# Kernel tuning notes

Measured on AMD Instinct MI355X. Metric: run time of the kernel, lower is better.

Reference implementation:

```python
import jax, jax.numpy as jnp
import numpy as np

B, S, I, H = 64, 2048, 256, 512

def setup_inputs() -> dict:
    key = jax.random.key(0)
    k1, k2, k3, k4 = jax.random.split(key, 4)
    stdv = 1.0 / np.sqrt(H)
    return {
        "x": jax.random.normal(k1, (B, S, I), dtype=jnp.float32),
        "W": jax.random.uniform(k2, (I, 3 * H), dtype=jnp.float32, minval=-stdv, maxval=stdv),
        "U": jax.random.uniform(k3, (H, 3 * H), dtype=jnp.float32, minval=-stdv, maxval=stdv),
        "bias": jax.random.uniform(k4, (3 * H,), dtype=jnp.float32, minval=-stdv, maxval=stdv),
    }

def _lstm_noforget(x, W, U, bias):
    # Precompute input projections for all timesteps: (B, S, 3H)
    x_proj = jnp.einsum("bsi,ig->bsg", x, W) + bias
    h0 = jnp.zeros((x.shape[0], H), dtype=x.dtype)
    c0 = jnp.zeros((x.shape[0], H), dtype=x.dtype)

    def step(carry, xp_t):
        h_t, _ = carry
        gates = xp_t + h_t @ U  # (B, 3H)
        i_t = jax.nn.sigmoid(gates[:, :H])
        g_t = jnp.tanh(gates[:, H:2 * H])
        o_t = jax.nn.sigmoid(gates[:, 2 * H:])
        c_t = i_t * g_t          # no-forget: c does not depend on previous c
        h_t = o_t * jnp.tanh(c_t)
        return (h_t, c_t), h_t

    (h_f, c_f), hs = jax.lax.scan(step, (h0, c0), jnp.swapaxes(x_proj, 0, 1))
    hidden_seq = jnp.swapaxes(hs, 0, 1)  # (B, S, H)
    return hidden_seq, h_f, c_f

def reference(x, W, U, bias):
    return _lstm_noforget(x, W, U, bias)
```

## Files before the change

kernel.cpp:

```cpp
#include <hip/hip_runtime.h>
#include <math.h>

#define B_  64
#define S_  2048
#define I_  256
#define H_  512
#define K_  768
#define G3  1536

#define RT  16
#define JT  4
#define NC  12
#define BLK 192
#define LDA 772

__global__ __launch_bounds__(256) void prep_transpose(
    const float* __restrict__ W,
    const float* __restrict__ U,
    float* __restrict__ Vt)
{
    const int c = blockIdx.y;
    const int k = blockIdx.x * 256 + threadIdx.x;
    if (k < K_) {
        float v = (k < I_) ? W[(size_t)k * G3 + c] : U[(size_t)(k - I_) * G3 + c];
        Vt[(size_t)c * K_ + k] = v;
    }
}

__global__ __launch_bounds__(BLK) void lstm_step(
    const float* __restrict__ x,
    const float* __restrict__ bias,
    const float* __restrict__ Vt,
    const float* __restrict__ h_in,
    float* __restrict__ h_out,
    float* __restrict__ hidden,
    float* __restrict__ hf,
    float* __restrict__ cf,
    int t, int is_last)
{
    __shared__ float Alds[RT * LDA];
    __shared__ float gtile[NC][RT + 1];

    const int tid = threadIdx.x;
    const int rq  = blockIdx.x & 3;
    const int jq  = blockIdx.x >> 2;
    const int r0  = rq * RT;

    for (int f4 = tid; f4 < (RT * I_) / 4; f4 += BLK) {
        const int r  = f4 >> 6;
        const int kk = (f4 & 63) * 4;
        const float4 v = *(const float4*)(x + (size_t)(r0 + r) * (S_ * I_) + (size_t)t * I_ + kk);
        *(float4*)(Alds + r * LDA + kk) = v;
    }
    for (int f4 = tid; f4 < (RT * H_) / 4; f4 += BLK) {
        const int r  = f4 >> 7;
        const int jj = (f4 & 127) * 4;
        const float4 v = *(const float4*)(h_in + (size_t)(r0 + r) * H_ + jj);
        *(float4*)(Alds + r * LDA + I_ + jj) = v;
    }
    __syncthreads();

    const int r      = tid & 15;
    const int c      = tid >> 4;
    const int region = c >> 2;
    const int jl     = c & 3;
    const int j      = jq * JT + jl;
    const int cg     = region * H_ + j;

    const float* __restrict__ wrow = Vt + (size_t)cg * K_;
    const float* __restrict__ arow = Alds + r * LDA;

    float4 acc = make_float4(0.f, 0.f, 0.f, 0.f);
    #pragma unroll 4
    for (int k = 0; k < K_; k += 8) {
        const float4 a0 = *(const float4*)(arow + k);
        const float4 a1 = *(const float4*)(arow + k + 4);
        const float4 w0 = *(const float4*)(wrow + k);
        const float4 w1 = *(const float4*)(wrow + k + 4);
        acc.x += a0.x * w0.x;  acc.y += a0.y * w0.y;
        acc.z += a0.z * w0.z;  acc.w += a0.w * w0.w;
        acc.x += a1.x * w1.x;  acc.y += a1.y * w1.y;
        acc.z += a1.z * w1.z;  acc.w += a1.w * w1.w;
    }
    gtile[c][r] = (acc.x + acc.y) + (acc.z + acc.w) + bias[cg];
    __syncthreads();

    if (tid < RT * JT) {
        const int rr = tid & 15;
        const int jj = tid >> 4;
        const float gi = gtile[0 * JT + jj][rr];
        const float gg = gtile[1 * JT + jj][rr];
        const float go = gtile[2 * JT + jj][rr];
        const float it = 1.f / (1.f + __expf(-gi));
        const float gt = tanhf(gg);
        const float ot = 1.f / (1.f + __expf(-go));
        const float ct = it * gt;
        const float ht = ot * tanhf(ct);
        const int rg = r0 + rr;
        const int jg = jq * JT + jj;
        h_out[(size_t)rg * H_ + jg] = ht;
        hidden[(size_t)rg * (S_ * H_) + (size_t)t * H_ + jg] = ht;
        if (is_last) {
            hf[(size_t)rg * H_ + jg] = ht;
            cf[(size_t)rg * H_ + jg] = ct;
        }
    }
}

extern "C" void kernel_launch(void* const* d_in, const int* in_sizes, int n_in,
                              void* d_out, int out_size, void* d_ws, size_t ws_size,
                              hipStream_t stream) {
    const float* x    = (const float*)d_in[0];
    const float* W    = (const float*)d_in[1];
    const float* U    = (const float*)d_in[2];
    const float* bias = (const float*)d_in[3];

    float* out    = (float*)d_out;
    float* hidden = out;
    float* hf     = out + (size_t)B_ * S_ * H_;
    float* cf     = hf + (size_t)B_ * H_;

    float* Vt = (float*)d_ws;
    float* h0 = Vt + (size_t)G3 * K_;
    float* h1 = h0 + (size_t)B_ * H_;

    hipLaunchKernelGGL(prep_transpose, dim3(3, G3), dim3(256), 0, stream, W, U, Vt);
    hipMemsetAsync(h0, 0, (size_t)B_ * H_ * sizeof(float), stream);

    float* hin = h0;
    float* hout = h1;
    for (int t = 0; t < S_; ++t) {
        hipLaunchKernelGGL(lstm_step, dim3(512), dim3(BLK), 0, stream,
                           x, bias, Vt, hin, hout, hidden, hf, cf, t, (t == S_ - 1) ? 1 : 0);
        float* tmp = hin; hin = hout; hout = tmp;
    }
}
```

Baseline: 33.04 ms.

## Replace per-step launches with persistent bf16 MFMA kernel and atomic group sync

Replaces the 2048 per-timestep kernel launches with a single persistent kernel of 128 workgroups. Each workgroup keeps its slice of the weights resident in LDS as bf16 and computes the gates with MFMA bf16 instructions. Steps are synchronized through per-batch-group atomic counters in global memory, and the x projection for the next step is computed while other groups finish. The aim is to remove launch overhead and repeated weight reloads. In exchange it introduces bf16 rounding of h and weights, relies on all workgroups being co-resident, and spin-waits on atomics.

```diff
diff --git a/kernel.cpp b/kernel.cpp
--- a/kernel.cpp
+++ b/kernel.cpp
@@ -1,108 +1,185 @@
 #include <hip/hip_runtime.h>
 #include <math.h>
 
-#define B_  64
-#define S_  2048
-#define I_  256
-#define H_  512
-#define K_  768
-#define G3  1536
-
-#define RT  16
-#define JT  4
-#define NC  12
-#define BLK 192
-#define LDA 772
-
-__global__ __launch_bounds__(256) void prep_transpose(
-    const float* __restrict__ W,
-    const float* __restrict__ U,
-    float* __restrict__ Vt)
-{
-    const int c = blockIdx.y;
-    const int k = blockIdx.x * 256 + threadIdx.x;
-    if (k < K_) {
-        float v = (k < I_) ? W[(size_t)k * G3 + c] : U[(size_t)(k - I_) * G3 + c];
-        Vt[(size_t)c * K_ + k] = v;
-    }
-}
-
-__global__ __launch_bounds__(BLK) void lstm_step(
+#define B_   64
+#define S_   2048
+#define I_   256
+#define H_   512
+#define K_   768
+#define G3   1536
+
+#define NTHR 384
+#define NWG  128
+#define AST  776
+
+typedef __attribute__((ext_vector_type(8))) short  s8v;
+typedef __attribute__((ext_vector_type(4))) float  f4v;
+
+static __device__ __forceinline__ unsigned short f2bf(float f) {
+    unsigned u = __float_as_uint(f);
+    return (unsigned short)((u + 0x7FFFu + ((u >> 16) & 1u)) >> 16);
+}
+static __device__ __forceinline__ float sigm(float v) { return 1.f / (1.f + __expf(-v)); }
+static __device__ __forceinline__ float tanh_(float v) {
+    float e = __expf(2.f * v);
+    return 1.f - 2.f / (e + 1.f);
+}
+
+__global__ __launch_bounds__(256) void prep_w(const float* __restrict__ W,
+                                              const float* __restrict__ U,
+                                              unsigned short* __restrict__ Wb) {
+    __shared__ float T[64][65];
+    const int kb = blockIdx.x * 64;
+    const int cb = blockIdx.y * 64;
+    const int tc = threadIdx.x & 63;
+    const int tg = threadIdx.x >> 6;
+    for (int rr = 0; rr < 16; ++rr) {
+        const int kl = tg * 16 + rr;
+        const int k  = kb + kl, c = cb + tc;
+        const float v = (k < I_) ? W[(size_t)k * G3 + c] : U[(size_t)(k - I_) * G3 + c];
+        T[tc][kl] = v;
+    }
+    __syncthreads();
+    for (int rr = 0; rr < 16; ++rr) {
+        const int cl = tg * 16 + rr;
+        Wb[(size_t)(cb + cl) * K_ + kb + tc] = f2bf(T[cl][tc]);
+    }
+}
+
+__global__ __launch_bounds__(NTHR, 1) void lstm_persist(
     const float* __restrict__ x,
     const float* __restrict__ bias,
-    const float* __restrict__ Vt,
-    const float* __restrict__ h_in,
-    float* __restrict__ h_out,
-    float* __restrict__ hidden,
-    float* __restrict__ hf,
-    float* __restrict__ cf,
-    int t, int is_last)
+    const unsigned short* __restrict__ Wb,
+    unsigned short* __restrict__ hex,
+    unsigned int* __restrict__ ctr,
+    float* __restrict__ hidden, float* __restrict__ hf, float* __restrict__ cf)
 {
-    __shared__ float Alds[RT * LDA];
-    __shared__ float gtile[NC][RT + 1];
-
-    const int tid = threadIdx.x;
-    const int rq  = blockIdx.x & 3;
-    const int jq  = blockIdx.x >> 2;
-    const int r0  = rq * RT;
-
-    for (int f4 = tid; f4 < (RT * I_) / 4; f4 += BLK) {
-        const int r  = f4 >> 6;
-        const int kk = (f4 & 63) * 4;
-        const float4 v = *(const float4*)(x + (size_t)(r0 + r) * (S_ * I_) + (size_t)t * I_ + kk);
-        *(float4*)(Alds + r * LDA + kk) = v;
-    }
-    for (int f4 = tid; f4 < (RT * H_) / 4; f4 += BLK) {
-        const int r  = f4 >> 7;
-        const int jj = (f4 & 127) * 4;
-        const float4 v = *(const float4*)(h_in + (size_t)(r0 + r) * H_ + jj);
-        *(float4*)(Alds + r * LDA + I_ + jj) = v;
+    __shared__ __align__(16) unsigned short Alds[16 * AST];
+    __shared__ __align__(16) unsigned short Wlds[48 * AST];
+    __shared__ float Glds[3][16][17];
+    __shared__ float bl[48];
+
+    const int tid  = threadIdx.x;
+    const int lane = tid & 63;
+    const int wv   = tid >> 6;
+    const int nt   = wv >> 1;
+    const int kp   = wv & 1;
+    const int mrow = lane & 15;
+    const int quad = lane >> 4;
+
+    const int bid = blockIdx.x;
+    const int g   = bid & 3;
+    const int cw  = bid >> 2;
+    const int r0  = g * 16;
+    const int j0  = cw * 16;
+    unsigned int* ctrg = ctr + g * 16;
+
+    unsigned short* hex0 = hex;
+    unsigned short* hex1 = hex + 64 * H_;
+
+    for (int q = tid; q < 48 * 96; q += NTHR) {
+        const int cl = q / 96, c16 = q % 96;
+        const int cg = (cl >> 4) * H_ + j0 + (cl & 15);
+        *(uint4*)(Wlds + cl * AST + c16 * 8) = *(const uint4*)(Wb + (size_t)cg * K_ + c16 * 8);
+    }
+    if (tid < 48) bl[tid] = bias[(tid >> 4) * H_ + j0 + (tid & 15)];
+
+    for (int q = tid; q < 1024; q += NTHR) {
+        const int row = q >> 6, k4 = (q & 63) * 4;
+        const float4 v = *(const float4*)(x + ((size_t)(r0 + row) * S_ + 0) * I_ + k4);
+        unsigned long long pk = (unsigned long long)f2bf(v.x)
+                              | ((unsigned long long)f2bf(v.y) << 16)
+                              | ((unsigned long long)f2bf(v.z) << 32)
+                              | ((unsigned long long)f2bf(v.w) << 48);
+        *(unsigned long long*)(Alds + row * AST + k4) = pk;
     }
     __syncthreads();
 
-    const int r      = tid & 15;
-    const int c      = tid >> 4;
-    const int region = c >> 2;
-    const int jl     = c & 3;
-    const int j      = jq * JT + jl;
-    const int cg     = region * H_ + j;
-
-    const float* __restrict__ wrow = Vt + (size_t)cg * K_;
-    const float* __restrict__ arow = Alds + r * LDA;
-
-    float4 acc = make_float4(0.f, 0.f, 0.f, 0.f);
-    #pragma unroll 4
-    for (int k = 0; k < K_; k += 8) {
-        const float4 a0 = *(const float4*)(arow + k);
-        const float4 a1 = *(const float4*)(arow + k + 4);
-        const float4 w0 = *(const float4*)(wrow + k);
-        const float4 w1 = *(const float4*)(wrow + k + 4);
-        acc.x += a0.x * w0.x;  acc.y += a0.y * w0.y;
-        acc.z += a0.z * w0.z;  acc.w += a0.w * w0.w;
-        acc.x += a1.x * w1.x;  acc.y += a1.y * w1.y;
-        acc.z += a1.z * w1.z;  acc.w += a1.w * w1.w;
-    }
-    gtile[c][r] = (acc.x + acc.y) + (acc.z + acc.w) + bias[cg];
-    __syncthreads();
-
-    if (tid < RT * JT) {
-        const int rr = tid & 15;
-        const int jj = tid >> 4;
-        const float gi = gtile[0 * JT + jj][rr];
-        const float gg = gtile[1 * JT + jj][rr];
-        const float go = gtile[2 * JT + jj][rr];
-        const float it = 1.f / (1.f + __expf(-gi));
-        const float gt = tanhf(gg);
-        const float ot = 1.f / (1.f + __expf(-go));
-        const float ct = it * gt;
-        const float ht = ot * tanhf(ct);
-        const int rg = r0 + rr;
-        const int jg = jq * JT + jj;
-        h_out[(size_t)rg * H_ + jg] = ht;
-        hidden[(size_t)rg * (S_ * H_) + (size_t)t * H_ + jg] = ht;
-        if (is_last) {
-            hf[(size_t)rg * H_ + jg] = ht;
-            cf[(size_t)rg * H_ + jg] = ct;
+    f4v accX = {0.f, 0.f, 0.f, 0.f};
+    for (int kt = kp; kt < 8; kt += 2) {
+        s8v a = *(const s8v*)(Alds + mrow * AST + kt * 32 + quad * 8);
+        s8v b = *(const s8v*)(Wlds + (nt * 16 + mrow) * AST + kt * 32 + quad * 8);
+        accX = __builtin_amdgcn_mfma_f32_16x16x32_bf16(a, b, accX, 0, 0, 0);
+    }
+
+    for (int t = 0; t < S_; ++t) {
+        if (tid == 0) {
+            while (__hip_atomic_load(ctrg, __ATOMIC_ACQUIRE, __HIP_MEMORY_SCOPE_AGENT)
+                   < 32u * (unsigned)t)
+                __builtin_amdgcn_s_sleep(2);
+        }
+        __syncthreads();
+
+        const unsigned short* hsrc = (t & 1) ? hex1 : hex0;
+        for (int q = tid; q < 1024; q += NTHR) {
+            const int row = q >> 6, k8 = (q & 63) * 8;
+            *(uint4*)(Alds + row * AST + I_ + k8) =
+                *(const uint4*)(hsrc + (size_t)(r0 + row) * H_ + k8);
+        }
+        __syncthreads();
+
+        f4v accH = {0.f, 0.f, 0.f, 0.f};
+        for (int kt = 8 + kp; kt < 24; kt += 2) {
+            s8v a = *(const s8v*)(Alds + mrow * AST + kt * 32 + quad * 8);
+            s8v b = *(const s8v*)(Wlds + (nt * 16 + mrow) * AST + kt * 32 + quad * 8);
+            accH = __builtin_amdgcn_mfma_f32_16x16x32_bf16(a, b, accH, 0, 0, 0);
+        }
+
+        if (kp == 0) {
+            #pragma unroll
+            for (int r = 0; r < 4; ++r)
+                Glds[nt][quad * 4 + r][mrow] = accX[r] + accH[r];
+        }
+        __syncthreads();
+        if (kp == 1) {
+            #pragma unroll
+            for (int r = 0; r < 4; ++r)
+                Glds[nt][quad * 4 + r][mrow] += accX[r] + accH[r];
+        }
+        __syncthreads();
+
+        unsigned short* hdst = (t & 1) ? hex0 : hex1;
+        if (tid < 256) {
+            const int m = tid >> 4, j = tid & 15;
+            const float gi = Glds[0][m][j] + bl[j];
+            const float gg = Glds[1][m][j] + bl[16 + j];
+            const float go = Glds[2][m][j] + bl[32 + j];
+            const float it = sigm(gi);
+            const float gt = tanh_(gg);
+            const float ot = sigm(go);
+            const float ct = it * gt;
+            const float ht = ot * tanh_(ct);
+            hidden[((size_t)(r0 + m) * S_ + t) * H_ + j0 + j] = ht;
+            hdst[(size_t)(r0 + m) * H_ + j0 + j] = f2bf(ht);
+            if (t == S_ - 1) {
+                hf[(size_t)(r0 + m) * H_ + j0 + j] = ht;
+                cf[(size_t)(r0 + m) * H_ + j0 + j] = ct;
+            }
+        }
+        __threadfence();
+        __syncthreads();
+
+        if (tid == 0)
+            __hip_atomic_fetch_add(ctrg, 1u, __ATOMIC_RELEASE, __HIP_MEMORY_SCOPE_AGENT);
+
+        if (t + 1 < S_) {
+            for (int q = tid; q < 1024; q += NTHR) {
+                const int row = q >> 6, k4 = (q & 63) * 4;
+                const float4 v = *(const float4*)(x + ((size_t)(r0 + row) * S_ + (t + 1)) * I_ + k4);
+                unsigned long long pk = (unsigned long long)f2bf(v.x)
+                                      | ((unsigned long long)f2bf(v.y) << 16)
+                                      | ((unsigned long long)f2bf(v.z) << 32)
+                                      | ((unsigned long long)f2bf(v.w) << 48);
+                *(unsigned long long*)(Alds + row * AST + k4) = pk;
+            }
+            __syncthreads();
+            f4v ax = {0.f, 0.f, 0.f, 0.f};
+            for (int kt = kp; kt < 8; kt += 2) {
+                s8v a = *(const s8v*)(Alds + mrow * AST + kt * 32 + quad * 8);
+                s8v b = *(const s8v*)(Wlds + (nt * 16 + mrow) * AST + kt * 32 + quad * 8);
+                ax = __builtin_amdgcn_mfma_f32_16x16x32_bf16(a, b, ax, 0, 0, 0);
+            }
+            accX = ax;
         }
     }
 }
@@ -120,18 +197,12 @@
     float* hf     = out + (size_t)B_ * S_ * H_;
     float* cf     = hf + (size_t)B_ * H_;
 
-    float* Vt = (float*)d_ws;
-    float* h0 = Vt + (size_t)G3 * K_;
-    float* h1 = h0 + (size_t)B_ * H_;
-
-    hipLaunchKernelGGL(prep_transpose, dim3(3, G3), dim3(256), 0, stream, W, U, Vt);
-    hipMemsetAsync(h0, 0, (size_t)B_ * H_ * sizeof(float), stream);
-
-    float* hin = h0;
-    float* hout = h1;
-    for (int t = 0; t < S_; ++t) {
-        hipLaunchKernelGGL(lstm_step, dim3(512), dim3(BLK), 0, stream,
-                           x, bias, Vt, hin, hout, hidden, hf, cf, t, (t == S_ - 1) ? 1 : 0);
-        float* tmp = hin; hin = hout; hout = tmp;
-    }
-}
+    unsigned short* Wb  = (unsigned short*)d_ws;
+    unsigned short* hex = Wb + (size_t)G3 * K_;
+    unsigned int*   ctr = (unsigned int*)(hex + 2 * 64 * H_);
+
+    hipMemsetAsync(hex, 0, 2 * 64 * H_ * sizeof(unsigned short) + 256, stream);
+    hipLaunchKernelGGL(prep_w, dim3(12, 24), dim3(256), 0, stream, W, U, Wb);
+    hipLaunchKernelGGL(lstm_persist, dim3(NWG), dim3(NTHR), 0, stream,
+                       x, bias, Wb, hex, ctr, hidden, hf, cf);
+}
```

After: 39.60 ms. 19.9% more time.
